# Kernel tuning notes

Hardware: AMD Instinct MI355X
Metric: run time of the kernel (lower is better)

Reference implementation:

```python
import jax, jax.numpy as jnp
import numpy as np

K_OUTLIER = 16   # decomposition_topk default k
Q = 127.0        # int8 symmetric quant scale


def _quantize(mat):
    # per-row abs-max symmetric quantization; torch .to(int8) truncates toward
    # zero, which matches XLA's float->int convert semantics.
    mmax = jnp.max(jnp.abs(mat), axis=-1)                      # [...,]
    q = (mat * (Q / mmax)[..., None]).astype(jnp.int8)
    return q, mmax


def setup_inputs() -> dict:
    key = jax.random.key(0)
    k1, k2, k3 = jax.random.split(key, 3)
    B, I, O = 4096, 2048, 2048
    x = jax.random.normal(k1, (B, I), jnp.float32)
    weight = jax.random.normal(k2, (O, I), jnp.float32) * 0.02  # nn.Linear convention [out, in]
    bias = jax.random.normal(k3, (O,), jnp.float32) * 0.02
    return {"x": x, "weight": weight, "bias": bias}


def reference(x, weight, bias):
    # --- weight-side prep (done once in __init__ in the torch module) ---
    col_max = jnp.max(jnp.abs(weight), axis=0)                 # [I] abs-max per input column
    idx = jax.lax.top_k(col_max, K_OUTLIER)[1]                 # [k] outlier input columns
    w_unq = weight[:, idx].T                                   # [k, O] fp outlier weights
    w0 = weight.at[:, idx].set(0.0)                            # zero outlier columns
    w_q, w_max = _quantize(w0)                                 # int8 [O, I], fp [O]

    # --- activation side ---
    x_unq = x[:, idx]                                          # [B, k]
    x1 = x.at[:, idx].set(0.0)
    x_q, x_max = _quantize(x1)                                 # int8 [B, I], fp [B]

    # int8 matmul accumulated in int32 (MatMulInteger), then dequantize
    res_q_i32 = jnp.matmul(x_q.astype(jnp.int32), w_q.T.astype(jnp.int32))  # [B, O]
    mx = x_max[:, None] * w_max[None, :]                       # outer product of row/col maxes
    res_q = (res_q_i32.astype(jnp.float32) / (Q * Q)).astype(jnp.float16).astype(jnp.float32) * mx

    # fp outlier path + bias
    res_unq = x_unq @ w_unq + bias                             # [B, O]
    return res_q + res_unq
```

## Files before the change

kernel.cpp:

```cpp
#include <hip/hip_runtime.h>
#include <hip/hip_fp16.h>
#include <stdint.h>

#define I_DIM 2048
#define O_DIM 2048
#define B_DIM 4096
#define KOUT 16

typedef int i32x4 __attribute__((ext_vector_type(4)));
typedef int i32x16 __attribute__((ext_vector_type(16)));
typedef float f32x4 __attribute__((ext_vector_type(4)));
typedef float f32x16 __attribute__((ext_vector_type(16)));
typedef _Float16 f16x8 __attribute__((ext_vector_type(8)));

#define TO_LDS(p) ((__attribute__((address_space(3))) void*)(p))
#define TO_GLB(p) ((const __attribute__((address_space(1))) void*)(p))

__global__ void colmax_kernel(const float* __restrict__ W, float* __restrict__ cmp) {
  int j = blockIdx.x * 256 + threadIdx.x;
  int i0 = blockIdx.y * 64;
  float m = 0.0f;
  const float* p = W + (size_t)i0 * I_DIM + j;
#pragma unroll 8
  for (int i = 0; i < 64; ++i)
    m = fmaxf(m, fabsf(p[(size_t)i * I_DIM]));
  cmp[blockIdx.y * I_DIM + j] = m;
}

__global__ void topk_kernel(const float* __restrict__ cmp, int* __restrict__ idx,
                            float* __restrict__ keep) {
  int t = threadIdx.x;
  float v[8];
#pragma unroll
  for (int u = 0; u < 8; ++u) v[u] = 0.0f;
  for (int rc = 0; rc < 32; ++rc) {
    const float* row = cmp + rc * I_DIM;
#pragma unroll
    for (int u = 0; u < 8; ++u) v[u] = fmaxf(v[u], row[u * 256 + t]);
  }
  for (int j = t; j < I_DIM; j += 256) keep[j] = 1.0f;
  __shared__ float wm_[4];
  __shared__ int wi_[4];
  __shared__ int sel;
  for (int k = 0; k < KOUT; ++k) {
    float m = v[0]; int mi = 0;
#pragma unroll
    for (int u = 1; u < 8; ++u) if (v[u] > m) { m = v[u]; mi = u; }
    int gi = mi * 256 + t;
#pragma unroll
    for (int s = 32; s; s >>= 1) {
      float om = __shfl_down(m, s);
      int oi = __shfl_down(gi, s);
      if (om > m) { m = om; gi = oi; }
    }
    if ((t & 63) == 0) { wm_[t >> 6] = m; wi_[t >> 6] = gi; }
    __syncthreads();
    if (t == 0) {
      float bm = wm_[0]; int bi = wi_[0];
      for (int w2 = 1; w2 < 4; ++w2) if (wm_[w2] > bm) { bm = wm_[w2]; bi = wi_[w2]; }
      idx[k] = bi; keep[bi] = 0.0f; sel = bi;
    }
    __syncthreads();
    if (t == (sel & 255)) v[sel >> 8] = -1.0f;
  }
}

__global__ __launch_bounds__(256) void quant_kernel(
    const float* __restrict__ X, const float* __restrict__ W,
    const float* __restrict__ keep, const int* __restrict__ idx,
    signed char* __restrict__ xq, signed char* __restrict__ wq,
    float* __restrict__ xmax, float* __restrict__ wmax,
    _Float16* __restrict__ xunqh,
    _Float16* __restrict__ wunqh) {
  int b = blockIdx.x;
  int t = threadIdx.x;
  bool isW = b < O_DIM;
  int r = isW ? b : (b - O_DIM);
  const float* src = isW ? (W + (size_t)r * I_DIM) : (X + (size_t)r * I_DIM);
  const float4* s4 = (const float4*)src;
  const float4* k4 = (const float4*)keep;
  float4 v0 = s4[t], v1 = s4[t + 256];
  float4 k0 = k4[t], k1 = k4[t + 256];
  v0.x *= k0.x; v0.y *= k0.y; v0.z *= k0.z; v0.w *= k0.w;
  v1.x *= k1.x; v1.y *= k1.y; v1.z *= k1.z; v1.w *= k1.w;
  float m = fmaxf(fmaxf(fmaxf(fabsf(v0.x), fabsf(v0.y)), fmaxf(fabsf(v0.z), fabsf(v0.w))),
                  fmaxf(fmaxf(fabsf(v1.x), fabsf(v1.y)), fmaxf(fabsf(v1.z), fabsf(v1.w))));
#pragma unroll
  for (int s = 32; s; s >>= 1) m = fmaxf(m, __shfl_xor(m, s));
  __shared__ float red[4];
  if ((t & 63) == 0) red[t >> 6] = m;
  __syncthreads();
  m = fmaxf(fmaxf(red[0], red[1]), fmaxf(red[2], red[3]));
  float sc = 127.0f / m;
  unsigned p0 = (unsigned char)(signed char)(int)(v0.x * sc)
              | ((unsigned)(unsigned char)(signed char)(int)(v0.y * sc) << 8)
              | ((unsigned)(unsigned char)(signed char)(int)(v0.z * sc) << 16)
              | ((unsigned)(unsigned char)(signed char)(int)(v0.w * sc) << 24);
  unsigned p1 = (unsigned char)(signed char)(int)(v1.x * sc)
              | ((unsigned)(unsigned char)(signed char)(int)(v1.y * sc) << 8)
              | ((unsigned)(unsigned char)(signed char)(int)(v1.z * sc) << 16)
              | ((unsigned)(unsigned char)(signed char)(int)(v1.w * sc) << 24);
  unsigned* qout = (unsigned*)(isW ? (wq + (size_t)r * I_DIM) : (xq + (size_t)r * I_DIM));
  qout[t] = p0;
  qout[t + 256] = p1;
  if (t == 0) { if (isW) wmax[r] = m; else xmax[r] = m; }
  if (t < KOUT) {
    float ov = src[idx[t]];
    _Float16* u = isW ? (wunqh + (size_t)r * KOUT) : (xunqh + (size_t)r * KOUT);
    u[t] = (_Float16)ov;
  }
}

__global__ __launch_bounds__(256) void gemm_kernel(
    const signed char* __restrict__ Aq,
    const signed char* __restrict__ Bq,
    const float* __restrict__ xmaxg,
    const float* __restrict__ wmaxg,
    const _Float16* __restrict__ xunqh,
    const _Float16* __restrict__ wunqh,
    const float* __restrict__ biasg,
    float* __restrict__ out) {
  constexpr int N = O_DIM, K = I_DIM;
  __shared__ __align__(16) signed char smem[32768];
  signed char* As = smem;
  signed char* Bs = smem + 16384;

  const int tid = threadIdx.x;
  const int lane = tid & 63;
  const int wave = tid >> 6;
  const int h = lane >> 5;
  const int ln31 = lane & 31;
  const int wm = (wave & 1) * 64;
  const int wn = (wave >> 1) * 64;
  const int m0 = blockIdx.y * 128;
  const int n0 = blockIdx.x * 128;

  const signed char* srcA[4];
  const signed char* srcB[4];
#pragma unroll
  for (int s = 0; s < 4; ++s) {
    int f = (s * 4 + wave) * 64 + lane;
    int r = f >> 3;
    int g = (f & 7) ^ (r & 7);
    srcA[s] = Aq + (size_t)(m0 + r) * K + g * 16;
    srcB[s] = Bq + (size_t)(n0 + r) * K + g * 16;
  }

  const int rA0 = wm + ln31, rA1 = rA0 + 32;
  const int rB0 = wn + ln31, rB1 = rB0 + 32;
  const int oA0 = rA0 * 128, sA0 = rA0 & 7;
  const int oA1 = rA1 * 128, sA1 = rA1 & 7;
  const int oB0 = rB0 * 128, sB0 = rB0 & 7;
  const int oB1 = rB1 * 128, sB1 = rB1 & 7;

  f16x8 afh[2], bfh[2];
#pragma unroll
  for (int i = 0; i < 2; ++i)
    afh[i] = *(const f16x8*)(xunqh + (size_t)(m0 + wm + i * 32 + ln31) * KOUT + h * 8);
#pragma unroll
  for (int j = 0; j < 2; ++j)
    bfh[j] = *(const f16x8*)(wunqh + (size_t)(n0 + wn + j * 32 + ln31) * KOUT + h * 8);

  i32x16 acc[2][2] = {};

  for (int kt = 0; kt < K; kt += 128) {
#pragma unroll
    for (int s = 0; s < 4; ++s) {
      __builtin_amdgcn_global_load_lds(TO_GLB(srcA[s] + kt), TO_LDS(As + (s * 4 + wave) * 1024), 16, 0, 0);
      __builtin_amdgcn_global_load_lds(TO_GLB(srcB[s] + kt), TO_LDS(Bs + (s * 4 + wave) * 1024), 16, 0, 0);
    }
    __syncthreads();
#pragma unroll
    for (int st = 0; st < 4; ++st) {
      int lc = st * 2 + h;
      i32x4 a0 = *(const i32x4*)(As + oA0 + ((lc ^ sA0) << 4));
      i32x4 a1 = *(const i32x4*)(As + oA1 + ((lc ^ sA1) << 4));
      i32x4 b0 = *(const i32x4*)(Bs + oB0 + ((lc ^ sB0) << 4));
      i32x4 b1 = *(const i32x4*)(Bs + oB1 + ((lc ^ sB1) << 4));
      acc[0][0] = __builtin_amdgcn_mfma_i32_32x32x32_i8(a0, b0, acc[0][0], 0, 0, 0);
      acc[0][1] = __builtin_amdgcn_mfma_i32_32x32x32_i8(a0, b1, acc[0][1], 0, 0, 0);
      acc[1][0] = __builtin_amdgcn_mfma_i32_32x32x32_i8(a1, b0, acc[1][0], 0, 0, 0);
      acc[1][1] = __builtin_amdgcn_mfma_i32_32x32x32_i8(a1, b1, acc[1][1], 0, 0, 0);
    }
    __syncthreads();
  }

  const float recip = 1.0f / 16129.0f;
#pragma unroll
  for (int i = 0; i < 2; ++i) {
#pragma unroll
    for (int j = 0; j < 2; ++j) {
      int col = n0 + wn + j * 32 + ln31;
      float wmv = wmaxg[col];
      float bv = biasg[col];
      f32x16 c;
#pragma unroll
      for (int g = 0; g < 4; ++g) {
        int rbase = m0 + wm + i * 32 + g * 8 + h * 4;
        f32x4 xmv = *(const f32x4*)(xmaxg + rbase);
#pragma unroll
        for (int r = 0; r < 4; ++r) {
          float v = (float)acc[i][j][g * 4 + r] * recip;
          v = __half2float(__float2half(v));
          c[g * 4 + r] = v * (xmv[r] * wmv) + bv;
        }
      }
      c = __builtin_amdgcn_mfma_f32_32x32x16_f16(afh[i], bfh[j], c, 0, 0, 0);
#pragma unroll
      for (int g = 0; g < 4; ++g) {
        int rbase = m0 + wm + i * 32 + g * 8 + h * 4;
#pragma unroll
        for (int r = 0; r < 4; ++r)
          out[(size_t)(rbase + r) * N + col] = c[g * 4 + r];
      }
    }
  }
}

extern "C" void kernel_launch(void* const* d_in, const int* in_sizes, int n_in,
                              void* d_out, int out_size, void* d_ws, size_t ws_size,
                              hipStream_t stream) {
  const float* x    = (const float*)d_in[0];
  const float* w    = (const float*)d_in[1];
  const float* bias = (const float*)d_in[2];
  float* out = (float*)d_out;
  char* ws = (char*)d_ws;

  float* cm_part   = (float*)(ws + 0);
  int* idx         = (int*)(ws + 262144);
  float* keep      = (float*)(ws + 262272);
  float* w_max     = (float*)(ws + 270464);
  float* x_max     = (float*)(ws + 278656);
  _Float16* x_unqh = (_Float16*)(ws + 295040);
  _Float16* w_unqh = (_Float16*)(ws + 426112);
  signed char* w_q = (signed char*)(ws + 491648);
  signed char* x_q = (signed char*)(ws + 4685952);

  colmax_kernel<<<dim3(8, 32), 256, 0, stream>>>(w, cm_part);
  topk_kernel<<<1, 256, 0, stream>>>(cm_part, idx, keep);
  quant_kernel<<<O_DIM + B_DIM, 256, 0, stream>>>(x, w, keep, idx, x_q, w_q,
                                                  x_max, w_max, x_unqh, w_unqh);
  gemm_kernel<<<dim3(O_DIM / 128, B_DIM / 128), 256, 0, stream>>>(
      x_q, w_q, x_max, w_max, x_unqh, w_unqh, bias, out);
}
```

Baseline: 149.3 us.

## Fuse prep stages into one cooperative kernel and double-buffer GEMM LDS tiles

Merges column-max, top-k selection and quantization into a single cooperative kernel. Grid-wide syncs separate the phases, and every block redundantly computes the top-k into its own shared memory, then quantizes six rows. This removes three kernel launches and the global keep/idx round trips. The GEMM main loop now double-buffers LDS, prefetching the next K tile while the current one is computed, which doubles LDS use to 64KB per block and may reduce occupancy. Running top-k redundantly in all 1024 blocks adds serial work to every block, and the cooperative launch requires the whole grid to be resident at once.

```diff
diff --git a/kernel.cpp b/kernel.cpp
--- a/kernel.cpp
+++ b/kernel.cpp
@@ -1,6 +1,9 @@
 #include <hip/hip_runtime.h>
 #include <hip/hip_fp16.h>
+#include <hip/hip_cooperative_groups.h>
 #include <stdint.h>
+
+namespace cg = cooperative_groups;
 
 #define I_DIM 2048
 #define O_DIM 2048
@@ -16,37 +19,56 @@
 #define TO_LDS(p) ((__attribute__((address_space(3))) void*)(p))
 #define TO_GLB(p) ((const __attribute__((address_space(1))) void*)(p))
 
-__global__ void colmax_kernel(const float* __restrict__ W, float* __restrict__ cmp) {
-  int j = blockIdx.x * 256 + threadIdx.x;
-  int i0 = blockIdx.y * 64;
-  float m = 0.0f;
-  const float* p = W + (size_t)i0 * I_DIM + j;
-#pragma unroll 8
-  for (int i = 0; i < 64; ++i)
-    m = fmaxf(m, fabsf(p[(size_t)i * I_DIM]));
-  cmp[blockIdx.y * I_DIM + j] = m;
-}
-
-__global__ void topk_kernel(const float* __restrict__ cmp, int* __restrict__ idx,
-                            float* __restrict__ keep) {
-  int t = threadIdx.x;
-  float v[8];
-#pragma unroll
-  for (int u = 0; u < 8; ++u) v[u] = 0.0f;
-  for (int rc = 0; rc < 32; ++rc) {
-    const float* row = cmp + rc * I_DIM;
-#pragma unroll
-    for (int u = 0; u < 8; ++u) v[u] = fmaxf(v[u], row[u * 256 + t]);
-  }
-  for (int j = t; j < I_DIM; j += 256) keep[j] = 1.0f;
+__global__ __launch_bounds__(256, 4) void prep_kernel(
+    const float* __restrict__ X, const float* __restrict__ W,
+    signed char* __restrict__ xq, signed char* __restrict__ wq,
+    float* __restrict__ xmax, float* __restrict__ wmax,
+    _Float16* __restrict__ xunqh,
+    _Float16* __restrict__ wunqh,
+    float* __restrict__ cmp,
+    float* __restrict__ cm) {
+  cg::grid_group grid = cg::this_grid();
+  const int b = blockIdx.x;
+  const int t = threadIdx.x;
+
+  {
+    int chunk = b >> 3;
+    int col = (b & 7) * 256 + t;
+    const float* p = W + (size_t)(chunk * 16) * I_DIM + col;
+    float m = 0.0f;
+#pragma unroll
+    for (int i = 0; i < 16; ++i) m = fmaxf(m, fabsf(p[(size_t)i * I_DIM]));
+    cmp[chunk * I_DIM + col] = m;
+  }
+  grid.sync();
+
+  if (b < 8) {
+    int col = b * 256 + t;
+    float m = 0.0f;
+    for (int c = 0; c < 128; ++c) m = fmaxf(m, cmp[c * I_DIM + col]);
+    cm[col] = m;
+  }
+  grid.sync();
+
+  __shared__ float keep[I_DIM];
+  __shared__ int idxs[KOUT];
   __shared__ float wm_[4];
   __shared__ int wi_[4];
   __shared__ int sel;
+  __shared__ float red[4];
+  float v[8];
+  {
+    const float4* c4 = (const float4*)cm;
+    float4 a4 = c4[t * 2], b4 = c4[t * 2 + 1];
+    v[0] = a4.x; v[1] = a4.y; v[2] = a4.z; v[3] = a4.w;
+    v[4] = b4.x; v[5] = b4.y; v[6] = b4.z; v[7] = b4.w;
+  }
+  for (int j = t; j < I_DIM; j += 256) keep[j] = 1.0f;
   for (int k = 0; k < KOUT; ++k) {
     float m = v[0]; int mi = 0;
 #pragma unroll
     for (int u = 1; u < 8; ++u) if (v[u] > m) { m = v[u]; mi = u; }
-    int gi = mi * 256 + t;
+    int gi = t * 8 + mi;
 #pragma unroll
     for (int s = 32; s; s >>= 1) {
       float om = __shfl_down(m, s);
@@ -58,56 +80,48 @@
     if (t == 0) {
       float bm = wm_[0]; int bi = wi_[0];
       for (int w2 = 1; w2 < 4; ++w2) if (wm_[w2] > bm) { bm = wm_[w2]; bi = wi_[w2]; }
-      idx[k] = bi; keep[bi] = 0.0f; sel = bi;
-    }
-    __syncthreads();
-    if (t == (sel & 255)) v[sel >> 8] = -1.0f;
-  }
-}
-
-__global__ __launch_bounds__(256) void quant_kernel(
-    const float* __restrict__ X, const float* __restrict__ W,
-    const float* __restrict__ keep, const int* __restrict__ idx,
-    signed char* __restrict__ xq, signed char* __restrict__ wq,
-    float* __restrict__ xmax, float* __restrict__ wmax,
-    _Float16* __restrict__ xunqh,
-    _Float16* __restrict__ wunqh) {
-  int b = blockIdx.x;
-  int t = threadIdx.x;
-  bool isW = b < O_DIM;
-  int r = isW ? b : (b - O_DIM);
-  const float* src = isW ? (W + (size_t)r * I_DIM) : (X + (size_t)r * I_DIM);
-  const float4* s4 = (const float4*)src;
+      idxs[k] = bi; keep[bi] = 0.0f; sel = bi;
+    }
+    __syncthreads();
+    if (t == (sel >> 3)) v[sel & 7] = -1.0f;
+  }
+
   const float4* k4 = (const float4*)keep;
-  float4 v0 = s4[t], v1 = s4[t + 256];
-  float4 k0 = k4[t], k1 = k4[t + 256];
-  v0.x *= k0.x; v0.y *= k0.y; v0.z *= k0.z; v0.w *= k0.w;
-  v1.x *= k1.x; v1.y *= k1.y; v1.z *= k1.z; v1.w *= k1.w;
-  float m = fmaxf(fmaxf(fmaxf(fabsf(v0.x), fabsf(v0.y)), fmaxf(fabsf(v0.z), fabsf(v0.w))),
-                  fmaxf(fmaxf(fabsf(v1.x), fabsf(v1.y)), fmaxf(fabsf(v1.z), fabsf(v1.w))));
-#pragma unroll
-  for (int s = 32; s; s >>= 1) m = fmaxf(m, __shfl_xor(m, s));
-  __shared__ float red[4];
-  if ((t & 63) == 0) red[t >> 6] = m;
-  __syncthreads();
-  m = fmaxf(fmaxf(red[0], red[1]), fmaxf(red[2], red[3]));
-  float sc = 127.0f / m;
-  unsigned p0 = (unsigned char)(signed char)(int)(v0.x * sc)
-              | ((unsigned)(unsigned char)(signed char)(int)(v0.y * sc) << 8)
-              | ((unsigned)(unsigned char)(signed char)(int)(v0.z * sc) << 16)
-              | ((unsigned)(unsigned char)(signed char)(int)(v0.w * sc) << 24);
-  unsigned p1 = (unsigned char)(signed char)(int)(v1.x * sc)
-              | ((unsigned)(unsigned char)(signed char)(int)(v1.y * sc) << 8)
-              | ((unsigned)(unsigned char)(signed char)(int)(v1.z * sc) << 16)
-              | ((unsigned)(unsigned char)(signed char)(int)(v1.w * sc) << 24);
-  unsigned* qout = (unsigned*)(isW ? (wq + (size_t)r * I_DIM) : (xq + (size_t)r * I_DIM));
-  qout[t] = p0;
-  qout[t + 256] = p1;
-  if (t == 0) { if (isW) wmax[r] = m; else xmax[r] = m; }
-  if (t < KOUT) {
-    float ov = src[idx[t]];
-    _Float16* u = isW ? (wunqh + (size_t)r * KOUT) : (xunqh + (size_t)r * KOUT);
-    u[t] = (_Float16)ov;
+  for (int i = 0; i < 6; ++i) {
+    int rid = b * 6 + i;
+    bool isW = rid < O_DIM;
+    int r = isW ? rid : rid - O_DIM;
+    const float* src = isW ? (W + (size_t)r * I_DIM) : (X + (size_t)r * I_DIM);
+    const float4* s4 = (const float4*)src;
+    float4 v0 = s4[t * 2], v1 = s4[t * 2 + 1];
+    float4 k0 = k4[t * 2], k1 = k4[t * 2 + 1];
+    v0.x *= k0.x; v0.y *= k0.y; v0.z *= k0.z; v0.w *= k0.w;
+    v1.x *= k1.x; v1.y *= k1.y; v1.z *= k1.z; v1.w *= k1.w;
+    float m = fmaxf(fmaxf(fmaxf(fabsf(v0.x), fabsf(v0.y)), fmaxf(fabsf(v0.z), fabsf(v0.w))),
+                    fmaxf(fmaxf(fabsf(v1.x), fabsf(v1.y)), fmaxf(fabsf(v1.z), fabsf(v1.w))));
+#pragma unroll
+    for (int s = 32; s; s >>= 1) m = fmaxf(m, __shfl_xor(m, s));
+    if ((t & 63) == 0) red[t >> 6] = m;
+    __syncthreads();
+    m = fmaxf(fmaxf(red[0], red[1]), fmaxf(red[2], red[3]));
+    float sc = 127.0f / m;
+    unsigned p0 = (unsigned char)(signed char)(int)(v0.x * sc)
+                | ((unsigned)(unsigned char)(signed char)(int)(v0.y * sc) << 8)
+                | ((unsigned)(unsigned char)(signed char)(int)(v0.z * sc) << 16)
+                | ((unsigned)(unsigned char)(signed char)(int)(v0.w * sc) << 24);
+    unsigned p1 = (unsigned char)(signed char)(int)(v1.x * sc)
+                | ((unsigned)(unsigned char)(signed char)(int)(v1.y * sc) << 8)
+                | ((unsigned)(unsigned char)(signed char)(int)(v1.z * sc) << 16)
+                | ((unsigned)(unsigned char)(signed char)(int)(v1.w * sc) << 24);
+    uint2* qout = (uint2*)(isW ? (wq + (size_t)r * I_DIM) : (xq + (size_t)r * I_DIM));
+    qout[t] = make_uint2(p0, p1);
+    if (t == 0) { if (isW) wmax[r] = m; else xmax[r] = m; }
+    if (t < KOUT) {
+      float ov = src[idxs[t]];
+      _Float16* u = isW ? (wunqh + (size_t)r * KOUT) : (xunqh + (size_t)r * KOUT);
+      u[t] = (_Float16)ov;
+    }
+    __syncthreads();
   }
 }
 
@@ -121,9 +135,7 @@
     const float* __restrict__ biasg,
     float* __restrict__ out) {
   constexpr int N = O_DIM, K = I_DIM;
-  __shared__ __align__(16) signed char smem[32768];
-  signed char* As = smem;
-  signed char* Bs = smem + 16384;
+  __shared__ __align__(16) signed char smem[65536];
 
   const int tid = threadIdx.x;
   const int lane = tid & 63;
@@ -163,13 +175,26 @@
 
   i32x16 acc[2][2] = {};
 
-  for (int kt = 0; kt < K; kt += 128) {
-#pragma unroll
-    for (int s = 0; s < 4; ++s) {
-      __builtin_amdgcn_global_load_lds(TO_GLB(srcA[s] + kt), TO_LDS(As + (s * 4 + wave) * 1024), 16, 0, 0);
-      __builtin_amdgcn_global_load_lds(TO_GLB(srcB[s] + kt), TO_LDS(Bs + (s * 4 + wave) * 1024), 16, 0, 0);
-    }
-    __syncthreads();
+#pragma unroll
+  for (int s = 0; s < 4; ++s) {
+    __builtin_amdgcn_global_load_lds(TO_GLB(srcA[s]), TO_LDS(smem + (s * 4 + wave) * 1024), 16, 0, 0);
+    __builtin_amdgcn_global_load_lds(TO_GLB(srcB[s]), TO_LDS(smem + 16384 + (s * 4 + wave) * 1024), 16, 0, 0);
+  }
+  __syncthreads();
+
+  for (int it = 0; it < K / 128; ++it) {
+    const int cur = (it & 1) * 32768;
+    const int nxt = cur ^ 32768;
+    if (it + 1 < K / 128) {
+      int kt = (it + 1) * 128;
+#pragma unroll
+      for (int s = 0; s < 4; ++s) {
+        __builtin_amdgcn_global_load_lds(TO_GLB(srcA[s] + kt), TO_LDS(smem + nxt + (s * 4 + wave) * 1024), 16, 0, 0);
+        __builtin_amdgcn_global_load_lds(TO_GLB(srcB[s] + kt), TO_LDS(smem + nxt + 16384 + (s * 4 + wave) * 1024), 16, 0, 0);
+      }
+    }
+    const signed char* As = smem + cur;
+    const signed char* Bs = smem + cur + 16384;
 #pragma unroll
     for (int st = 0; st < 4; ++st) {
       int lc = st * 2 + h;
@@ -226,20 +251,20 @@
   float* out = (float*)d_out;
   char* ws = (char*)d_ws;
 
-  float* cm_part   = (float*)(ws + 0);
-  int* idx         = (int*)(ws + 262144);
-  float* keep      = (float*)(ws + 262272);
-  float* w_max     = (float*)(ws + 270464);
-  float* x_max     = (float*)(ws + 278656);
-  _Float16* x_unqh = (_Float16*)(ws + 295040);
-  _Float16* w_unqh = (_Float16*)(ws + 426112);
-  signed char* w_q = (signed char*)(ws + 491648);
-  signed char* x_q = (signed char*)(ws + 4685952);
-
-  colmax_kernel<<<dim3(8, 32), 256, 0, stream>>>(w, cm_part);
-  topk_kernel<<<1, 256, 0, stream>>>(cm_part, idx, keep);
-  quant_kernel<<<O_DIM + B_DIM, 256, 0, stream>>>(x, w, keep, idx, x_q, w_q,
-                                                  x_max, w_max, x_unqh, w_unqh);
+  float* cmp       = (float*)(ws + 0);
+  float* cm        = (float*)(ws + 1048576);
+  float* w_max     = (float*)(ws + 1056768);
+  float* x_max     = (float*)(ws + 1064960);
+  _Float16* x_unqh = (_Float16*)(ws + 1081344);
+  _Float16* w_unqh = (_Float16*)(ws + 1212416);
+  signed char* w_q = (signed char*)(ws + 1277952);
+  signed char* x_q = (signed char*)(ws + 5472256);
+
+  void* args[] = {(void*)&x, (void*)&w, (void*)&x_q, (void*)&w_q,
+                  (void*)&x_max, (void*)&w_max, (void*)&x_unqh, (void*)&w_unqh,
+                  (void*)&cmp, (void*)&cm};
+  hipLaunchCooperativeKernel((void*)prep_kernel, dim3(1024), dim3(256), args, 0, stream);
+
   gemm_kernel<<<dim3(O_DIM / 128, B_DIM / 128), 256, 0, stream>>>(
       x_q, w_q, x_max, w_max, x_unqh, w_unqh, bias, out);
 }
```

New measurement: 337.1 us. 2.26x slower.
